# Optimization experiments

Hardware: AMD Instinct MI355X
Metric: run time of the kernel (lower is better)

Reference implementation:

```python
import jax, jax.numpy as jnp
import numpy as np

DIM = 512
NUM_HEADS = 8
HEAD_DIM = DIM // NUM_HEADS
SR = 2
LN_EPS = 1e-5


def setup_inputs() -> dict:
    key = jax.random.key(0)
    ks = jax.random.split(key, 12)
    B, H, W = 8, 32, 32
    N = H * W
    s = 0.02
    return {
        "x": jax.random.normal(ks[0], (B, N, DIM), jnp.float32),
        "H": H,
        "W": W,
        # weights stored as [in, out] (torch Linear applies x @ W.T + b)
        "q_w": jax.random.normal(ks[1], (DIM, DIM), jnp.float32) * s,
        "q_b": jnp.zeros((DIM,), jnp.float32),
        "kv_w": jax.random.normal(ks[2], (DIM, 2 * DIM), jnp.float32) * s,
        "kv_b": jnp.zeros((2 * DIM,), jnp.float32),
        "sr_w": jax.random.normal(ks[3], (DIM, DIM, SR, SR), jnp.float32) * s,  # OIHW
        "sr_b": jnp.zeros((DIM,), jnp.float32),
        "ln_g": jnp.ones((DIM,), jnp.float32),
        "ln_b": jnp.zeros((DIM,), jnp.float32),
        "proj_w": jax.random.normal(ks[4], (DIM, DIM), jnp.float32) * s,
        "proj_b": jnp.zeros((DIM,), jnp.float32),
    }


def reference(x, H, W, q_w, q_b, kv_w, kv_b, sr_w, sr_b, ln_g, ln_b, proj_w, proj_b):
    B, N, C = x.shape
    hd = HEAD_DIM
    scale = hd ** -0.5

    # q: [B, nh, N, hd]
    q = (x @ q_w + q_b).reshape(B, N, NUM_HEADS, hd).transpose(0, 2, 1, 3)

    # spatial reduction conv (stride=kernel=SR) + LayerNorm
    x2d = x.transpose(0, 2, 1).reshape(B, C, H, W)
    x2d = jax.lax.conv_general_dilated(
        x2d, sr_w, window_strides=(SR, SR), padding="VALID",
        dimension_numbers=("NCHW", "OIHW", "NCHW")) + sr_b[None, :, None, None]
    Nk = x2d.shape[2] * x2d.shape[3]
    x_kv = x2d.reshape(B, C, Nk).transpose(0, 2, 1)  # [B, Nk, C]
    mu = x_kv.mean(-1, keepdims=True)
    var = ((x_kv - mu) ** 2).mean(-1, keepdims=True)
    x_kv = (x_kv - mu) * jax.lax.rsqrt(var + LN_EPS) * ln_g + ln_b

    kv = x_kv @ kv_w + kv_b  # [B, Nk, 2C]
    k, v = kv[..., :C], kv[..., C:]
    # Faithful to torch: reshape folds C/hd into kv-sequence axis -> M = Nk*num_heads,
    # shared (broadcast) across all query heads.
    M = Nk * NUM_HEADS
    k = k.reshape(B, M, hd)
    v = v.reshape(B, M, hd)

    attn = jnp.einsum("bhnd,bmd->bhnm", q, k) * scale  # [B, nh, N, M]
    attn = jax.nn.softmax(attn, axis=-1)
    out = jnp.einsum("bhnm,bmd->bhnd", attn, v)  # [B, nh, N, hd]
    out = out.transpose(0, 2, 1, 3).reshape(B, N, C)
    return out @ proj_w + proj_b
```

## Files before the change

### kernel.cpp

```cpp
#include <hip/hip_runtime.h>
#include <hip/hip_bf16.h>
#include <stdint.h>

typedef __attribute__((ext_vector_type(8))) short short8;
typedef __attribute__((ext_vector_type(4))) float f32x4;

#define MFMA(A, B, C) __builtin_amdgcn_mfma_f32_16x16x32_bf16(A, B, C, 0, 0, 0)

__device__ inline uint32_t bfrne(float f) {
  uint32_t u = __float_as_uint(f);
  return (u + 0x7FFFu + ((u >> 16) & 1u)) >> 16;
}

__device__ inline uint32_t pkrne(float a, float b) {
  union { __hip_bfloat162 v; uint32_t u; } c;
  c.v.x = __float2bfloat16(a);
  c.v.y = __float2bfloat16(b);
  return c.u;
}

__device__ inline float fexp2(float x) { return __builtin_amdgcn_exp2f(x); }

__device__ inline void gload16(const short* g, short* l) {
  __builtin_amdgcn_global_load_lds(
      (const __attribute__((address_space(1))) void*)g,
      (__attribute__((address_space(3))) void*)l, 16, 0, 0);
}

__global__ __launch_bounds__(256) void prep_all_kernel(
    const float* __restrict__ sr_w, const float* __restrict__ kv_w,
    const float* __restrict__ q_w, const float* __restrict__ proj_w,
    const float* __restrict__ x,
    short* __restrict__ WcThi, short* __restrict__ kvThi,
    short* __restrict__ qThi, short* __restrict__ pThi,
    short* __restrict__ xhi) {
  __shared__ float tile[32][33];
  const int blk = blockIdx.x;
  if (blk < 4096) {
    int t = blk * 256 + threadIdx.x;
    int kk = t & 2047, o = t >> 11;
    float v = sr_w[(size_t)o * 2048 + ((kk & 511) << 2) + (kk >> 9)];
    WcThi[t] = (short)bfrne(v);
    return;
  }
  if (blk >= 5120) {
    int t = (blk - 5120) * 256 + threadIdx.x;
    float4 v0 = *(const float4*)&x[(size_t)t * 8];
    float4 v1 = *(const float4*)&x[(size_t)t * 8 + 4];
    uint4 pk;
    pk.x = pkrne(v0.x, v0.y);
    pk.y = pkrne(v0.z, v0.w);
    pk.z = pkrne(v1.x, v1.y);
    pk.w = pkrne(v1.z, v1.w);
    *(uint4*)&xhi[(size_t)t * 8] = pk;
    return;
  }
  const float* in; short* ohi; int N, bx, by;
  if (blk < 4608) {
    in = kv_w; ohi = kvThi; N = 1024;
    int i = blk - 4096; bx = i & 31; by = i >> 5;
  } else if (blk < 4864) {
    in = q_w; ohi = qThi; N = 512;
    int i = blk - 4608; bx = i & 15; by = i >> 4;
  } else {
    in = proj_w; ohi = pThi; N = 512;
    int i = blk - 4864; bx = i & 15; by = i >> 4;
  }
  const int K = 512;
  const int tx = threadIdx.x & 31, ty = threadIdx.x >> 5;
#pragma unroll
  for (int i = 0; i < 4; ++i)
    tile[ty + i * 8][tx] = in[(size_t)(by * 32 + ty + i * 8) * N + bx * 32 + tx];
  __syncthreads();
#pragma unroll
  for (int i = 0; i < 4; ++i) {
    int n = bx * 32 + ty + i * 8;
    float v = tile[tx][ty + i * 8];
    ohi[(size_t)n * K + by * 32 + tx] = (short)bfrne(v);
  }
}

__global__ __launch_bounds__(256) void ln_kernel(
    const float* __restrict__ X, const float* __restrict__ g,
    const float* __restrict__ bta, short* __restrict__ hi) {
  const int row = blockIdx.x, t = threadIdx.x;
  size_t idx = (size_t)row * 512 + t * 2;
  const size_t PS = (size_t)2048 * 512;
  float2 a0 = *(const float2*)&X[idx];
  float2 a1 = *(const float2*)&X[idx + PS];
  float2 a2 = *(const float2*)&X[idx + 2 * PS];
  float2 a3 = *(const float2*)&X[idx + 3 * PS];
  float x0 = a0.x + a1.x + a2.x + a3.x;
  float x1 = a0.y + a1.y + a2.y + a3.y;
  float s = x0 + x1, sq = x0 * x0 + x1 * x1;
#pragma unroll
  for (int off = 1; off < 64; off <<= 1) {
    s += __shfl_xor(s, off);
    sq += __shfl_xor(sq, off);
  }
  __shared__ float rs[4], rq[4];
  int wid = t >> 6;
  if ((t & 63) == 0) { rs[wid] = s; rq[wid] = sq; }
  __syncthreads();
  s = rs[0] + rs[1] + rs[2] + rs[3];
  sq = rq[0] + rq[1] + rq[2] + rq[3];
  float mu = s * (1.f / 512), var = sq * (1.f / 512) - mu * mu;
  float inv = rsqrtf(var + 1e-5f);
  float2 gg = *(const float2*)&g[t * 2], bb = *(const float2*)&bta[t * 2];
  float o0 = (x0 - mu) * inv * gg.x + bb.x;
  float o1 = (x1 - mu) * inv * gg.y + bb.y;
  *(uint32_t*)&hi[idx] = pkrne(o0, o1);
}

__global__ void kv_post_kernel(const float* __restrict__ KV1, const float* __restrict__ KV2,
                               short* __restrict__ Kf, short* __restrict__ Vf) {
  const int blk = blockIdx.x;
  if (blk < 4096) {
    int t = blk * 256 + threadIdx.x;
    int j = t & 7, l = (t >> 3) & 63, i = (t >> 9) & 7, tt = (t >> 12) & 31, b = t >> 17;
    int qi = l & 15, g = l >> 4, h2 = i & 1, mf = i >> 1;
    int m = tt * 64 + mf * 16 + qi, d = h2 * 32 + g * 8 + j;
    size_t idx = ((size_t)b * 256 + (m >> 3)) * 1024 + (m & 7) * 64 + d;
    Kf[t] = (short)bfrne(KV1[idx] + KV2[idx]);
  } else {
    int t = (blk - 4096) * 256 + threadIdx.x;
    int j = t & 7, l = (t >> 3) & 63, i = (t >> 9) & 7, tt = (t >> 12) & 31, b = t >> 17;
    int qi = l & 15, g = l >> 4, df = i & 3, ks2 = i >> 2;
    int mm = tt * 64 + ks2 * 32 + g * 8 + j, dd = df * 16 + qi;
    size_t idx = ((size_t)b * 256 + (mm >> 3)) * 1024 + 512 + (mm & 7) * 64 + dd;
    Vf[t] = (short)bfrne(KV1[idx] + KV2[idx]);
  }
}

template <bool GATHER, int OMODE>
__device__ __forceinline__ void gemm_body(
    short* ldsraw,
    const short* __restrict__ Ahi, const short* __restrict__ BThi,
    const float* __restrict__ bias, float* __restrict__ C,
    short* __restrict__ Chi, float oscale,
    int M, int N, int lda, int ldb, int klen,
    int bxx, int byy, int bzz) {
  typedef short (*ldsA_t)[64][8];
  typedef short (*ldsB_t)[128][8];
  ldsA_t ldsA = (ldsA_t)ldsraw;
  ldsB_t ldsB = (ldsB_t)(ldsraw + 8 * 64 * 8);
  const int tid = threadIdx.x, lane = tid & 63, wave = tid >> 6;
  const int g = lane >> 4, qi = lane & 15;
  const int row0 = bxx * 64, col0 = byy * 128;
  const int kz = bzz * klen;
  float* Cz = C + (size_t)bzz * M * N;
  const bool dobias = (bzz == 0);
  f32x4 acc[4][2] = {};

  for (int k0 = kz; k0 < kz + klen; k0 += 64) {
    __syncthreads();
#pragma unroll
    for (int r = 0; r < 2; ++r) {
      int c = tid + r * 256;
      int arow = c & 63, akg = c >> 6;
      size_t ao;
      if (GATHER) {
        int row = row0 + arow;
        int bi = row >> 8, p = row & 255;
        int col = k0 + akg * 8;
        int seg = col >> 9, cc = col & 511;
        int n = (2 * (p >> 4) + (seg >> 1)) * 32 + 2 * (p & 15) + (seg & 1);
        ao = ((size_t)bi * 1024 + n) * 512 + cc;
      } else {
        ao = (size_t)(row0 + arow) * lda + k0 + akg * 8;
      }
      gload16(&Ahi[ao], &ldsA[akg][arow][0]);
    }
#pragma unroll
    for (int r = 0; r < 4; ++r) {
      int c = tid + r * 256;
      int bcol = c & 127, bkg = c >> 7;
      size_t bo = (size_t)(col0 + bcol) * ldb + k0 + bkg * 8;
      gload16(&BThi[bo], &ldsB[bkg][bcol][0]);
    }
    __syncthreads();
#pragma unroll
    for (int kk = 0; kk < 2; ++kk) {
      const int kg = kk * 4 + g;
      short8 ah[4], bh[2];
#pragma unroll
      for (int i = 0; i < 4; ++i)
        ah[i] = *(const short8*)&ldsA[kg][i * 16 + qi][0];
#pragma unroll
      for (int j = 0; j < 2; ++j)
        bh[j] = *(const short8*)&ldsB[kg][wave * 32 + j * 16 + qi][0];
#pragma unroll
      for (int i = 0; i < 4; ++i)
#pragma unroll
        for (int j = 0; j < 2; ++j)
          acc[i][j] = MFMA(ah[i], bh[j], acc[i][j]);
    }
  }
#pragma unroll
  for (int i = 0; i < 4; ++i)
#pragma unroll
    for (int j = 0; j < 2; ++j) {
      int colb = col0 + wave * 32 + j * 16 + qi;
      float bs = dobias ? bias[colb] : 0.f;
#pragma unroll
      for (int r = 0; r < 4; ++r) {
        int row = row0 + i * 16 + g * 4 + r;
        if (OMODE == 0) {
          Cz[(size_t)row * N + colb] = acc[i][j][r] + bs;
        } else {
          Chi[(size_t)row * N + colb] = (short)bfrne((acc[i][j][r] + bs) * oscale);
        }
      }
    }
}

template <bool GATHER, int OMODE>
__global__ __launch_bounds__(256) void gemm_1p(
    const short* __restrict__ Ahi, const short* __restrict__ BThi,
    const float* __restrict__ bias, float* __restrict__ C,
    short* __restrict__ Chi, float oscale,
    int M, int N, int lda, int ldb, int klen) {
  __shared__ short lds[12288];
  gemm_body<GATHER, OMODE>(lds, Ahi, BThi, bias, C, Chi, oscale,
                           M, N, lda, ldb, klen,
                           blockIdx.x, blockIdx.y, blockIdx.z);
}

__global__ __launch_bounds__(256) void conv_q_kernel(
    const short* __restrict__ xhi, const short* __restrict__ WcThi,
    const float* __restrict__ sr_b, float* __restrict__ Cbuf,
    const short* __restrict__ qThi, const float* __restrict__ q_b,
    short* __restrict__ Qhi, float qscale) {
  __shared__ short lds[12288];
  const int blk = blockIdx.x;
  if (blk < 512) {
    int bx = blk & 31, by = (blk >> 5) & 3, bz = blk >> 7;
    gemm_body<true, 0>(lds, xhi, WcThi, sr_b, Cbuf, nullptr, 1.f,
                       2048, 512, 512, 2048, 512, bx, by, bz);
  } else {
    int i = blk - 512;
    int bx = i & 127, by = i >> 7;
    gemm_body<false, 1>(lds, xhi, qThi, q_b, nullptr, Qhi, qscale,
                        8192, 512, 512, 512, 512, bx, by, 0);
  }
}

__device__ __forceinline__ void ld8(short8 (&dst)[8], const short* base) {
#pragma unroll
  for (int i = 0; i < 8; ++i)
    dst[i] = *(const short8*)&base[(size_t)i * 512];
}

__device__ __forceinline__ void qk_tile(f32x4 (&s)[2][4], const short8 (&kr)[8],
                                        const short8 (&qh)[2][2]) {
  const f32x4 z = {0.f, 0.f, 0.f, 0.f};
  __builtin_amdgcn_s_setprio(1);
#pragma unroll
  for (int mf = 0; mf < 4; ++mf)
#pragma unroll
    for (int qc = 0; qc < 2; ++qc) {
      s[qc][mf] = MFMA(kr[mf * 2 + 0], qh[qc][0], z);
      s[qc][mf] = MFMA(kr[mf * 2 + 1], qh[qc][1], s[qc][mf]);
    }
  __builtin_amdgcn_s_setprio(0);
}

__device__ __forceinline__ void pack_tile(const f32x4 (&s)[2][4], short* Psw,
                                          int g, int qi, int swz) {
#pragma unroll
  for (int qc = 0; qc < 2; ++qc)
#pragma unroll
    for (int mf = 0; mf < 4; ++mf) {
      uint32_t u0 = __float_as_uint(fexp2(s[qc][mf][0]));
      uint32_t u1 = __float_as_uint(fexp2(s[qc][mf][1]));
      uint32_t u2 = __float_as_uint(fexp2(s[qc][mf][2]));
      uint32_t u3 = __float_as_uint(fexp2(s[qc][mf][3]));
      uint2 hp;
      hp.x = (u0 >> 16) | (u1 & 0xffff0000u);
      hp.y = (u2 >> 16) | (u3 & 0xffff0000u);
      int uw = ((mf * 4 + g) ^ swz) << 2;
      *(uint2*)&Psw[qc * 1024 + qi * 64 + uw] = hp;
    }
}

__device__ __forceinline__ void pv_tile(const short8 (&vr)[8], short* Psw,
                                        f32x4 (&lacc)[2], f32x4 (&oacc)[2][4],
                                        int g, int qi, int swz) {
  const short8 ones = {(short)0x3F80, (short)0x3F80, (short)0x3F80, (short)0x3F80,
                       (short)0x3F80, (short)0x3F80, (short)0x3F80, (short)0x3F80};
#pragma unroll
  for (int qc = 0; qc < 2; ++qc)
#pragma unroll
    for (int ks2 = 0; ks2 < 2; ++ks2) {
      int ur = ((ks2 * 8 + g * 2) ^ swz) << 2;
      short8 pa = *(const short8*)&Psw[qc * 1024 + qi * 64 + ur];
      __builtin_amdgcn_s_setprio(1);
      lacc[qc] = MFMA(ones, pa, lacc[qc]);
#pragma unroll
      for (int df = 0; df < 4; ++df)
        oacc[qc][df] = MFMA(vr[ks2 * 4 + df], pa, oacc[qc][df]);
      __builtin_amdgcn_s_setprio(0);
    }
}

__global__ __launch_bounds__(256, 2) void attn_kernel(
    const short* __restrict__ Qhi, const short* __restrict__ Kf,
    const short* __restrict__ Vf, short* __restrict__ Ohi) {
  __shared__ short Ps[4][2][1024];
  const int tid = threadIdx.x, lane = tid & 63, wave = tid >> 6;
  const int g = lane >> 4, qi = lane & 15;
  const int h = blockIdx.y, b = blockIdx.z;
  const int n0 = blockIdx.x * 128 + wave * 32;
  const int swz = (qi & 7) << 1;
  short* Psw = &Ps[wave][0][0];

  short8 qh[2][2];
#pragma unroll
  for (int qc = 0; qc < 2; ++qc) {
    const size_t qrow = ((size_t)b * 1024 + n0 + qc * 16 + qi) * 512 + h * 64;
#pragma unroll
    for (int ks = 0; ks < 2; ++ks)
      qh[qc][ks] = *(const short8*)&Qhi[qrow + (ks * 4 + g) * 8];
  }
  f32x4 lacc[2] = {};
  f32x4 oacc[2][4] = {};
  const short* Kb = Kf + (size_t)b * 131072 + lane * 8;
  const short* Vb = Vf + (size_t)b * 131072 + lane * 8;

  short8 kA[8], kB[8], vr[8];
  f32x4 sA[2][4], sB[2][4];
  ld8(kA, Kb);
  ld8(kB, Kb + 4096);
  qk_tile(sA, kA, qh);
  for (int t = 0; t < 32; t += 2) {
    const short* tK = Kb + (size_t)t * 4096;
    const short* tV = Vb + (size_t)t * 4096;
    ld8(vr, tV);
    if (t < 30) ld8(kA, tK + 8192);
    pack_tile(sA, Psw, g, qi, swz);
    qk_tile(sB, kB, qh);
    pv_tile(vr, Psw, lacc, oacc, g, qi, swz);
    ld8(vr, tV + 4096);
    if (t < 30) ld8(kB, tK + 12288);
    pack_tile(sB, Psw, g, qi, swz);
    if (t < 30) qk_tile(sA, kA, qh);
    pv_tile(vr, Psw, lacc, oacc, g, qi, swz);
  }
#pragma unroll
  for (int qc = 0; qc < 2; ++qc) {
    float linv = 1.f / lacc[qc][0];
    size_t obase = ((size_t)b * 1024 + n0 + qc * 16 + qi) * 512 + h * 64;
#pragma unroll
    for (int df = 0; df < 4; ++df) {
      float o0 = oacc[qc][df][0] * linv, o1 = oacc[qc][df][1] * linv;
      float o2 = oacc[qc][df][2] * linv, o3 = oacc[qc][df][3] * linv;
      uint2 hp;
      hp.x = pkrne(o0, o1);
      hp.y = pkrne(o2, o3);
      *(uint2*)&Ohi[obase + df * 16 + g * 4] = hp;
    }
  }
}

extern "C" void kernel_launch(void* const* d_in, const int* in_sizes, int n_in,
                              void* d_out, int out_size, void* d_ws, size_t ws_size,
                              hipStream_t stream) {
  const float* x      = (const float*)d_in[0];
  const float* q_w    = (const float*)d_in[3];
  const float* q_b    = (const float*)d_in[4];
  const float* kv_w   = (const float*)d_in[5];
  const float* kv_b   = (const float*)d_in[6];
  const float* sr_w   = (const float*)d_in[7];
  const float* sr_b   = (const float*)d_in[8];
  const float* ln_g   = (const float*)d_in[9];
  const float* ln_b   = (const float*)d_in[10];
  const float* proj_w = (const float*)d_in[11];
  const float* proj_b = (const float*)d_in[12];

  char* W = (char*)d_ws;
  const size_t MB = 1024 * 1024;
  short* xhi   = (short*)(W);
  short* WcThi = (short*)(W + 16 * MB);
  float* Cbuf  = (float*)(W + 20 * MB);
  short* LNhi  = (short*)(W + 36 * MB);
  short* kvThi = (short*)(W + 40 * MB);
  short* qThi  = (short*)(W + 42 * MB);
  short* pThi  = (short*)(W + 43 * MB);
  short* Qhi   = (short*)(W + 44 * MB);
  float* KVp   = (float*)(W + 20 * MB);
  short* Kf    = (short*)(W + 36 * MB);
  short* Vf    = (short*)(W + 16 * MB);
  short* Ohi   = (short*)(W);

  prep_all_kernel<<<7168, 256, 0, stream>>>(
      sr_w, kv_w, q_w, proj_w, x, WcThi, kvThi, qThi, pThi, xhi);
  conv_q_kernel<<<1024, 256, 0, stream>>>(
      xhi, WcThi, sr_b, Cbuf, qThi, q_b, Qhi, 0.125f * 1.44269504f);
  ln_kernel<<<2048, 256, 0, stream>>>(Cbuf, ln_g, ln_b, LNhi);
  gemm_1p<false, 0><<<dim3(32, 8, 2), 256, 0, stream>>>(
      LNhi, kvThi, kv_b, KVp, nullptr, 1.f, 2048, 1024, 512, 512, 256);
  kv_post_kernel<<<8192, 256, 0, stream>>>(KVp, KVp + (size_t)2 * MB, Kf, Vf);
  attn_kernel<<<dim3(8, 8, 8), 256, 0, stream>>>(Qhi, Kf, Vf, Ohi);
  gemm_1p<false, 0><<<dim3(128, 4, 1), 256, 0, stream>>>(
      Ohi, pThi, proj_b, (float*)d_out, nullptr, 1.f, 8192, 512, 512, 512, 512);
}
```

Before: 125.9 us.

## Fuse KV post-processing into KV GEMM epilogue and drop split-K

The KV projection GEMM now writes bf16 K and V straight into the fragment-swizzled layouts the attention kernel expects, so the separate kv_post kernel and its fp32 partial buffers go away. Split-K with two partials is replaced by one full-K pass with a 256-block grid. This removes a launch and the fp32 write/read round trip. In exchange the GEMM has half as many blocks and its epilogue stores are scattered 2-byte writes.

New measurement: 118.7 us. 1.06x faster.

```diff
diff --git a/kernel.cpp b/kernel.cpp
--- a/kernel.cpp
+++ b/kernel.cpp
@@ -112,32 +112,12 @@
   *(uint32_t*)&hi[idx] = pkrne(o0, o1);
 }
 
-__global__ void kv_post_kernel(const float* __restrict__ KV1, const float* __restrict__ KV2,
-                               short* __restrict__ Kf, short* __restrict__ Vf) {
-  const int blk = blockIdx.x;
-  if (blk < 4096) {
-    int t = blk * 256 + threadIdx.x;
-    int j = t & 7, l = (t >> 3) & 63, i = (t >> 9) & 7, tt = (t >> 12) & 31, b = t >> 17;
-    int qi = l & 15, g = l >> 4, h2 = i & 1, mf = i >> 1;
-    int m = tt * 64 + mf * 16 + qi, d = h2 * 32 + g * 8 + j;
-    size_t idx = ((size_t)b * 256 + (m >> 3)) * 1024 + (m & 7) * 64 + d;
-    Kf[t] = (short)bfrne(KV1[idx] + KV2[idx]);
-  } else {
-    int t = (blk - 4096) * 256 + threadIdx.x;
-    int j = t & 7, l = (t >> 3) & 63, i = (t >> 9) & 7, tt = (t >> 12) & 31, b = t >> 17;
-    int qi = l & 15, g = l >> 4, df = i & 3, ks2 = i >> 2;
-    int mm = tt * 64 + ks2 * 32 + g * 8 + j, dd = df * 16 + qi;
-    size_t idx = ((size_t)b * 256 + (mm >> 3)) * 1024 + 512 + (mm & 7) * 64 + dd;
-    Vf[t] = (short)bfrne(KV1[idx] + KV2[idx]);
-  }
-}
-
 template <bool GATHER, int OMODE>
 __device__ __forceinline__ void gemm_body(
     short* ldsraw,
     const short* __restrict__ Ahi, const short* __restrict__ BThi,
     const float* __restrict__ bias, float* __restrict__ C,
-    short* __restrict__ Chi, float oscale,
+    short* __restrict__ Chi, short* __restrict__ Vfo, float oscale,
     int M, int N, int lda, int ldb, int klen,
     int bxx, int byy, int bzz) {
   typedef short (*ldsA_t)[64][8];
@@ -207,8 +187,25 @@
         int row = row0 + i * 16 + g * 4 + r;
         if (OMODE == 0) {
           Cz[(size_t)row * N + colb] = acc[i][j][r] + bs;
+        } else if (OMODE == 1) {
+          Chi[(size_t)row * N + colb] = (short)bfrne((acc[i][j][r] + bs) * oscale);
         } else {
-          Chi[(size_t)row * N + colb] = (short)bfrne((acc[i][j][r] + bs) * oscale);
+          uint32_t hv = bfrne(acc[i][j][r] + bs);
+          int bb2 = row >> 8, p = row & 255;
+          if (colb < 512) {
+            int m = p * 8 + (colb >> 6), d = colb & 63;
+            size_t t = ((((size_t)(bb2 * 32 + (m >> 6)) * 8 +
+                          ((m >> 4) & 3) * 2 + (d >> 5)) * 64) +
+                        ((d >> 3) & 3) * 16 + (m & 15)) * 8 + (d & 7);
+            Chi[t] = (short)hv;
+          } else {
+            int c2 = colb - 512;
+            int m = p * 8 + (c2 >> 6), d = c2 & 63;
+            size_t t = ((((size_t)(bb2 * 32 + (m >> 6)) * 8 +
+                          ((m >> 5) & 1) * 4 + (d >> 4)) * 64) +
+                        ((m >> 3) & 3) * 16 + (d & 15)) * 8 + (m & 7);
+            Vfo[t] = (short)hv;
+          }
         }
       }
     }
@@ -218,10 +215,10 @@
 __global__ __launch_bounds__(256) void gemm_1p(
     const short* __restrict__ Ahi, const short* __restrict__ BThi,
     const float* __restrict__ bias, float* __restrict__ C,
-    short* __restrict__ Chi, float oscale,
+    short* __restrict__ Chi, short* __restrict__ Vfo, float oscale,
     int M, int N, int lda, int ldb, int klen) {
   __shared__ short lds[12288];
-  gemm_body<GATHER, OMODE>(lds, Ahi, BThi, bias, C, Chi, oscale,
+  gemm_body<GATHER, OMODE>(lds, Ahi, BThi, bias, C, Chi, Vfo, oscale,
                            M, N, lda, ldb, klen,
                            blockIdx.x, blockIdx.y, blockIdx.z);
 }
@@ -235,12 +232,12 @@
   const int blk = blockIdx.x;
   if (blk < 512) {
     int bx = blk & 31, by = (blk >> 5) & 3, bz = blk >> 7;
-    gemm_body<true, 0>(lds, xhi, WcThi, sr_b, Cbuf, nullptr, 1.f,
+    gemm_body<true, 0>(lds, xhi, WcThi, sr_b, Cbuf, nullptr, nullptr, 1.f,
                        2048, 512, 512, 2048, 512, bx, by, bz);
   } else {
     int i = blk - 512;
     int bx = i & 127, by = i >> 7;
-    gemm_body<false, 1>(lds, xhi, qThi, q_b, nullptr, Qhi, qscale,
+    gemm_body<false, 1>(lds, xhi, qThi, q_b, nullptr, Qhi, nullptr, qscale,
                         8192, 512, 512, 512, 512, bx, by, 0);
   }
 }
@@ -387,9 +384,8 @@
   short* qThi  = (short*)(W + 42 * MB);
   short* pThi  = (short*)(W + 43 * MB);
   short* Qhi   = (short*)(W + 44 * MB);
-  float* KVp   = (float*)(W + 20 * MB);
-  short* Kf    = (short*)(W + 36 * MB);
-  short* Vf    = (short*)(W + 16 * MB);
+  short* Kf    = (short*)(W + 20 * MB);
+  short* Vf    = (short*)(W + 22 * MB);
   short* Ohi   = (short*)(W);
 
   prep_all_kernel<<<7168, 256, 0, stream>>>(
@@ -397,10 +393,10 @@
   conv_q_kernel<<<1024, 256, 0, stream>>>(
       xhi, WcThi, sr_b, Cbuf, qThi, q_b, Qhi, 0.125f * 1.44269504f);
   ln_kernel<<<2048, 256, 0, stream>>>(Cbuf, ln_g, ln_b, LNhi);
-  gemm_1p<false, 0><<<dim3(32, 8, 2), 256, 0, stream>>>(
-      LNhi, kvThi, kv_b, KVp, nullptr, 1.f, 2048, 1024, 512, 512, 256);
-  kv_post_kernel<<<8192, 256, 0, stream>>>(KVp, KVp + (size_t)2 * MB, Kf, Vf);
+  gemm_1p<false, 2><<<dim3(32, 8, 1), 256, 0, stream>>>(
+      LNhi, kvThi, kv_b, nullptr, Kf, Vf, 1.f, 2048, 1024, 512, 512, 512);
   attn_kernel<<<dim3(8, 8, 8), 256, 0, stream>>>(Qhi, Kf, Vf, Ohi);
   gemm_1p<false, 0><<<dim3(128, 4, 1), 256, 0, stream>>>(
-      Ohi, pThi, proj_b, (float*)d_out, nullptr, 1.f, 8192, 512, 512, 512, 512);
-}
+      Ohi, pThi, proj_b, (float*)d_out, nullptr, nullptr, 1.f,
+      8192, 512, 512, 512, 512);
+}
```
